# Kernel optimization log

Measured on AMD Instinct MI355X. Metric: run time of the kernel, lower is better.

Reference implementation:

```python
import jax, jax.numpy as jnp
import numpy as np

N = 20000
E = 320000
IN = 256
H = 4
C = 64
NEG_SLOPE = 0.2


def setup_inputs() -> dict:
    key = jax.random.key(0)
    ks = jax.random.split(key, 12)
    HC = H * C

    def w(k, shape, fan_in):
        return jax.random.normal(k, shape, dtype=jnp.float32) / np.sqrt(fan_in)

    x = jax.random.normal(ks[0], (N, IN), dtype=jnp.float32)
    edge_index = jax.random.randint(ks[1], (2, E), 0, N, dtype=jnp.int64)
    return {
        "x": x,
        "edge_index": edge_index,
        "Wl1": w(ks[2], (IN, HC), IN),
        "Wr1": w(ks[3], (IN, HC), IN),
        "att1": w(ks[4], (H, C), C),
        "b1": jnp.zeros((HC,), dtype=jnp.float32),
        "Wl2": w(ks[5], (HC, HC), HC),
        "Wr2": w(ks[6], (HC, HC), HC),
        "att2": w(ks[7], (H, C), C),
        "b2": jnp.zeros((HC,), dtype=jnp.float32),
        "Wfc": w(ks[8], (HC, 2), HC),
        "bfc": jnp.zeros((2,), dtype=jnp.float32),
    }


def _gatv2(x, src, dst, Wl, Wr, att, b):
    """GATv2Conv (concat=True, share_weights=False), inference (no dropout)."""
    n = x.shape[0]
    xl = (x @ Wl).reshape(n, H, C)  # source-side projection
    xr = (x @ Wr).reshape(n, H, C)  # target-side projection
    # per-edge GATv2 score: a^T LeakyReLU(xl_j + xr_i)
    e = jax.nn.leaky_relu(xl[src] + xr[dst], NEG_SLOPE)      # [E, H, C]
    score = jnp.einsum("ehc,hc->eh", e, att)                 # [E, H]
    # segment softmax over incoming edges of each target node
    smax = jax.ops.segment_max(score, dst, num_segments=n)   # [N, H]
    ex = jnp.exp(score - smax[dst])
    denom = jax.ops.segment_sum(ex, dst, num_segments=n)     # [N, H]
    alpha = ex / denom[dst]                                  # [E, H]
    # scatter-aggregate messages (source projections weighted by alpha)
    out = jax.ops.segment_sum(alpha[:, :, None] * xl[src], dst, num_segments=n)
    return out.reshape(n, H * C) + b


def reference(x, edge_index, Wl1, Wr1, att1, b1, Wl2, Wr2, att2, b2, Wfc, bfc):
    n = x.shape[0]
    # add_self_loops=True (PyG default)
    loop = jnp.arange(n, dtype=edge_index.dtype)
    src = jnp.concatenate([edge_index[0], loop])
    dst = jnp.concatenate([edge_index[1], loop])

    h = _gatv2(x, src, dst, Wl1, Wr1, att1, b1)
    h = jax.nn.relu(h)
    h = _gatv2(h, src, dst, Wl2, Wr2, att2, b2)
    h = jax.nn.relu(h)
    g = jnp.mean(h, axis=0, keepdims=True)  # [1, H*C]
    return g @ Wfc + bfc                    # [1, 2]
```

## Files before the change

kernel.cpp:

```cpp
#include <hip/hip_runtime.h>
#include <hip/hip_bf16.h>
#include <math.h>

#define Nn 20000
#define Ee 320000
#define INF_ 256
#define Hh 4
#define Cc 64
#define HC 256
#define NEG_SLOPE 0.2f

using frag16 = __attribute__((ext_vector_type(8))) short;
using f32x4  = __attribute__((ext_vector_type(4))) float;

__device__ __forceinline__ void async16(const void* g, void* l) {
    __builtin_amdgcn_global_load_lds(
        (const __attribute__((address_space(1))) unsigned int*)g,
        (__attribute__((address_space(3))) unsigned int*)l,
        16, 0, 0);
}


__global__ void init_deg(int* deg, int n) {
    int i = blockIdx.x * blockDim.x + threadIdx.x;
    if (i < n) deg[i] = 1;
}

__global__ void hist_kernel(const int* __restrict__ dst, int ne, int* deg) {
    int e = blockIdx.x * blockDim.x + threadIdx.x;
    if (e < ne) atomicAdd(&deg[dst[e]], 1);
}

__global__ __launch_bounds__(256) void scan1(const int* __restrict__ deg,
                                             int* __restrict__ excl,
                                             int* __restrict__ bsum, int n) {
    int tid = threadIdx.x;
    int gid = blockIdx.x * 256 + tid;
    int lane = tid & 63;
    int v = (gid < n) ? deg[gid] : 0;
    int x = v;
    #pragma unroll
    for (int off = 1; off < 64; off <<= 1) {
        int y = __shfl_up(x, off, 64);
        if (lane >= off) x += y;
    }
    __shared__ int wsum[4];
    if (lane == 63) wsum[tid >> 6] = x;
    __syncthreads();
    int wadd = 0;
    for (int w = 0; w < (tid >> 6); ++w) wadd += wsum[w];
    int incl = x + wadd;
    if (gid < n) excl[gid] = incl - v;
    if (tid == 255) bsum[blockIdx.x] = incl;
}

__global__ void scan2(const int* __restrict__ bsum, int* __restrict__ boff, int nb) {
    int lane = threadIdx.x;
    int carry = 0;
    for (int base = 0; base < nb; base += 64) {
        int i = base + lane;
        int v = (i < nb) ? bsum[i] : 0;
        int x = v;
        #pragma unroll
        for (int off = 1; off < 64; off <<= 1) {
            int y = __shfl_up(x, off, 64);
            if (lane >= off) x += y;
        }
        if (i < nb) boff[i] = carry + x - v;
        carry += __shfl(x, 63, 64);
    }
    if (lane == 0) boff[nb] = carry;
}

__global__ void scan_add(int* __restrict__ row_start, int* __restrict__ cursor,
                         const int* __restrict__ boff, int n, int nb) {
    int gid = blockIdx.x * blockDim.x + threadIdx.x;
    if (gid < n) {
        int v = row_start[gid] + boff[gid >> 8];
        row_start[gid] = v;
        cursor[gid] = v;
    }
    if (gid == n) row_start[n] = boff[nb];
}

__global__ void scatter_kernel(const int* __restrict__ src, const int* __restrict__ dst,
                               int ne, int n, int* cursor, int* colx) {
    int e = blockIdx.x * blockDim.x + threadIdx.x;
    if (e < ne) {
        int d = dst[e];
        int pos = atomicAdd(&cursor[d], 1);
        colx[pos] = src[e];
    } else if (e < ne + n) {
        int node = e - ne;
        int pos = atomicAdd(&cursor[node], 1);
        colx[pos] = node;
    }
}


__device__ inline unsigned short bf16rn(float f) {
    unsigned u = __float_as_uint(f);
    unsigned r = (u + 0x7FFFu + ((u >> 16) & 1u)) >> 16;
    return (unsigned short)r;
}

__device__ inline void split1(float v, short& h, short& l) {
    unsigned short hh = bf16rn(v);
    float back = __uint_as_float(((unsigned)hh) << 16);
    unsigned short ll = bf16rn(v - back);
    h = (short)hh; l = (short)ll;
}

__device__ __forceinline__ float4 bf4_to_f4(ushort4 u) {
    return make_float4(__uint_as_float((unsigned)u.x << 16),
                       __uint_as_float((unsigned)u.y << 16),
                       __uint_as_float((unsigned)u.z << 16),
                       __uint_as_float((unsigned)u.w << 16));
}

__global__ __launch_bounds__(256) void split_kernel(const float* __restrict__ in,
                                                    short* __restrict__ hi,
                                                    short* __restrict__ lo, int n4) {
    int i = blockIdx.x * blockDim.x + threadIdx.x;
    if (i >= n4) return;
    float4 v = ((const float4*)in)[i];
    short4 h, l;
    split1(v.x, h.x, l.x);
    split1(v.y, h.y, l.y);
    split1(v.z, h.z, l.z);
    split1(v.w, h.w, l.w);
    ((short4*)hi)[i] = h;
    ((short4*)lo)[i] = l;
}

__global__ __launch_bounds__(256) void wsplit_all(const float* __restrict__ Wl1,
                                                  const float* __restrict__ Wr1,
                                                  const float* __restrict__ Wl2,
                                                  const float* __restrict__ Wr2,
                                                  short* __restrict__ WhT1,
                                                  short* __restrict__ WlT1,
                                                  short* __restrict__ WhT2,
                                                  short* __restrict__ WlT2) {
    int b = blockIdx.x;
    int n = b & 255;
    int k = threadIdx.x;
    const float* W = (b < 256) ? Wl1 : (b < 512) ? Wr1 : (b < 768) ? Wl2 : Wr2;
    short* Wh = (b < 512) ? WhT1 : WhT2;
    short* Wl = (b < 512) ? WlT1 : WlT2;
    int col = b & 511;
    float v = W[k * 256 + n];
    short h, l;
    split1(v, h, l);
    Wh[col * 256 + k] = h;
    Wl[col * 256 + k] = l;
}


__global__ __launch_bounds__(256, 4) void mfma_gemm(const short* __restrict__ Ah,
                                                    const short* __restrict__ Al,
                                                    const short* __restrict__ WhT,
                                                    const short* __restrict__ WlT,
                                                    unsigned short* __restrict__ XLh,
                                                    float* __restrict__ XR) {
    __shared__ short BsH[64 * 256];
    __shared__ short BsL[64 * 256];

    int tid = threadIdx.x;
    int wave = tid >> 6, lane = tid & 63;
    int quad = lane >> 4, lc = lane & 15;

    int v = blockIdx.x;
    int p = (v & 7) * 157 + (v >> 3);
    int rowt = p >> 3;
    int colg = p & 7;
    int bm = rowt * 128;
    int cbase = (colg * 64) & 255;

    {
        int cl0 = wave * 2 + (lane >> 5);
        int kcs = (lane & 31) ^ (cl0 & 7);
        const short* srcH = WhT + (size_t)(colg * 64 + cl0) * HC + kcs * 8;
        const short* srcL = WlT + (size_t)(colg * 64 + cl0) * HC + kcs * 8;
        short* dstH = &BsH[wave * 512];
        short* dstL = &BsL[wave * 512];
        #pragma unroll
        for (int r = 0; r < 8; ++r) {
            async16(srcH + (size_t)r * 8 * HC, dstH + r * 2048);
            async16(srcL + (size_t)r * 8 * HC, dstL + r * 2048);
        }
    }

    int row0 = bm + wave * 32 + lc;
    int row1 = row0 + 16;
    int ca0 = (row0 < Nn) ? row0 : (Nn - 1);
    int ca1 = (row1 < Nn) ? row1 : (Nn - 1);
    const short* pa0h = Ah + (size_t)ca0 * HC + quad * 8;
    const short* pa1h = Ah + (size_t)ca1 * HC + quad * 8;
    const short* pa0l = Al + (size_t)ca0 * HC + quad * 8;
    const short* pa1l = Al + (size_t)ca1 * HC + quad * 8;

    __syncthreads();

    f32x4 acc[2][4] = {};
    #pragma unroll
    for (int c = 0; c < 8; ++c) {
        int k0 = c * 32;
        frag16 a0h = *(const frag16*)(pa0h + k0);
        frag16 a1h = *(const frag16*)(pa1h + k0);
        frag16 a0l = *(const frag16*)(pa0l + k0);
        frag16 a1l = *(const frag16*)(pa1l + k0);
        int sw = ((c * 4 + quad) ^ (lc & 7)) * 8;
        frag16 bh0 = *(const frag16*)&BsH[(0 * 16 + lc) * HC + sw];
        frag16 bh1 = *(const frag16*)&BsH[(1 * 16 + lc) * HC + sw];
        frag16 bh2 = *(const frag16*)&BsH[(2 * 16 + lc) * HC + sw];
        frag16 bh3 = *(const frag16*)&BsH[(3 * 16 + lc) * HC + sw];
        frag16 bl0 = *(const frag16*)&BsL[(0 * 16 + lc) * HC + sw];
        frag16 bl1 = *(const frag16*)&BsL[(1 * 16 + lc) * HC + sw];
        frag16 bl2 = *(const frag16*)&BsL[(2 * 16 + lc) * HC + sw];
        frag16 bl3 = *(const frag16*)&BsL[(3 * 16 + lc) * HC + sw];
        acc[0][0] = __builtin_amdgcn_mfma_f32_16x16x32_bf16(bh0, a0h, acc[0][0], 0, 0, 0);
        acc[1][0] = __builtin_amdgcn_mfma_f32_16x16x32_bf16(bh0, a1h, acc[1][0], 0, 0, 0);
        acc[0][1] = __builtin_amdgcn_mfma_f32_16x16x32_bf16(bh1, a0h, acc[0][1], 0, 0, 0);
        acc[1][1] = __builtin_amdgcn_mfma_f32_16x16x32_bf16(bh1, a1h, acc[1][1], 0, 0, 0);
        acc[0][2] = __builtin_amdgcn_mfma_f32_16x16x32_bf16(bh2, a0h, acc[0][2], 0, 0, 0);
        acc[1][2] = __builtin_amdgcn_mfma_f32_16x16x32_bf16(bh2, a1h, acc[1][2], 0, 0, 0);
        acc[0][3] = __builtin_amdgcn_mfma_f32_16x16x32_bf16(bh3, a0h, acc[0][3], 0, 0, 0);
        acc[1][3] = __builtin_amdgcn_mfma_f32_16x16x32_bf16(bh3, a1h, acc[1][3], 0, 0, 0);
        acc[0][0] = __builtin_amdgcn_mfma_f32_16x16x32_bf16(bh0, a0l, acc[0][0], 0, 0, 0);
        acc[1][0] = __builtin_amdgcn_mfma_f32_16x16x32_bf16(bh0, a1l, acc[1][0], 0, 0, 0);
        acc[0][1] = __builtin_amdgcn_mfma_f32_16x16x32_bf16(bh1, a0l, acc[0][1], 0, 0, 0);
        acc[1][1] = __builtin_amdgcn_mfma_f32_16x16x32_bf16(bh1, a1l, acc[1][1], 0, 0, 0);
        acc[0][2] = __builtin_amdgcn_mfma_f32_16x16x32_bf16(bh2, a0l, acc[0][2], 0, 0, 0);
        acc[1][2] = __builtin_amdgcn_mfma_f32_16x16x32_bf16(bh2, a1l, acc[1][2], 0, 0, 0);
        acc[0][3] = __builtin_amdgcn_mfma_f32_16x16x32_bf16(bh3, a0l, acc[0][3], 0, 0, 0);
        acc[1][3] = __builtin_amdgcn_mfma_f32_16x16x32_bf16(bh3, a1l, acc[1][3], 0, 0, 0);
        acc[0][0] = __builtin_amdgcn_mfma_f32_16x16x32_bf16(bl0, a0h, acc[0][0], 0, 0, 0);
        acc[1][0] = __builtin_amdgcn_mfma_f32_16x16x32_bf16(bl0, a1h, acc[1][0], 0, 0, 0);
        acc[0][1] = __builtin_amdgcn_mfma_f32_16x16x32_bf16(bl1, a0h, acc[0][1], 0, 0, 0);
        acc[1][1] = __builtin_amdgcn_mfma_f32_16x16x32_bf16(bl1, a1h, acc[1][1], 0, 0, 0);
        acc[0][2] = __builtin_amdgcn_mfma_f32_16x16x32_bf16(bl2, a0h, acc[0][2], 0, 0, 0);
        acc[1][2] = __builtin_amdgcn_mfma_f32_16x16x32_bf16(bl2, a1h, acc[1][2], 0, 0, 0);
        acc[0][3] = __builtin_amdgcn_mfma_f32_16x16x32_bf16(bl3, a0h, acc[0][3], 0, 0, 0);
        acc[1][3] = __builtin_amdgcn_mfma_f32_16x16x32_bf16(bl3, a1h, acc[1][3], 0, 0, 0);
    }

    #pragma unroll
    for (int mt = 0; mt < 2; ++mt) {
        int rw = bm + wave * 32 + mt * 16 + lc;
        if (rw >= Nn) continue;
        #pragma unroll
        for (int t = 0; t < 4; ++t) {
            int col0 = cbase + t * 16 + quad * 4;
            if (colg < 4) {
                ushort4 o;
                o.x = bf16rn(acc[mt][t][0]);
                o.y = bf16rn(acc[mt][t][1]);
                o.z = bf16rn(acc[mt][t][2]);
                o.w = bf16rn(acc[mt][t][3]);
                *(ushort4*)&XLh[(size_t)rw * HC + col0] = o;
            } else {
                *(f32x4*)&XR[(size_t)rw * HC + col0] = acc[mt][t];
            }
        }
    }
}


__device__ __forceinline__ float edge_score(const float4 v, const float4 xr,
                                            const float4 a06, const float4 a04) {
    float tx = v.x + xr.x, ty = v.y + xr.y, tz = v.z + xr.z, tw = v.w + xr.w;
    float p = a06.x * tx + a04.x * fabsf(tx);
    p += a06.y * ty + a04.y * fabsf(ty);
    p += a06.z * tz + a04.z * fabsf(tz);
    p += a06.w * tw + a04.w * fabsf(tw);
    p += __shfl_xor(p, 1, 64);
    p += __shfl_xor(p, 2, 64);
    p += __shfl_xor(p, 4, 64);
    p += __shfl_xor(p, 8, 64);
    return p;
}

__global__ __launch_bounds__(256) void gat_kernel(const ushort4* __restrict__ XL4,
                                                  const float4* __restrict__ XR4,
                                                  const int* __restrict__ row_start,
                                                  const int* __restrict__ colx,
                                                  const float4* __restrict__ att4,
                                                  const float4* __restrict__ bias4,
                                                  float4* __restrict__ Hout,
                                                  short4* __restrict__ Ahi,
                                                  short4* __restrict__ Alo,
                                                  int mode) {
    int wave = threadIdx.x >> 6, lane = threadIdx.x & 63;
    int node = blockIdx.x * 4 + wave;
    float4 xr = XR4[(size_t)node * 64 + lane];
    float4 a  = att4[lane];
    float4 a06 = make_float4(a.x * 0.6f, a.y * 0.6f, a.z * 0.6f, a.w * 0.6f);
    float4 a04 = make_float4(a.x * 0.4f, a.y * 0.4f, a.z * 0.4f, a.w * 0.4f);
    int e0 = __builtin_amdgcn_readfirstlane(row_start[node]);
    int e1 = __builtin_amdgcn_readfirstlane(row_start[node + 1]);
    float l0 = 0.f, l1 = 0.f;
    float4 acc0 = make_float4(0.f, 0.f, 0.f, 0.f);
    float4 acc1 = make_float4(0.f, 0.f, 0.f, 0.f);
    int npairs = (e1 - e0) >> 1;
    int e = e0;
    int s0 = 0, s1 = 0;
    if (npairs > 0) { s0 = colx[e]; s1 = colx[e + 1]; }
    for (int pp = 0; pp < npairs; ++pp) {
        int en = e + 2;
        int i0 = (en     < e1) ? en     : (e1 - 1);
        int i1 = (en + 1 < e1) ? en + 1 : (e1 - 1);
        int ns0 = colx[i0];
        int ns1 = colx[i1];
        ushort4 u0 = XL4[(size_t)s0 * 64 + lane];
        ushort4 u1 = XL4[(size_t)s1 * 64 + lane];
        float4 v0 = bf4_to_f4(u0);
        float4 v1 = bf4_to_f4(u1);
        float pe0 = __expf(edge_score(v0, xr, a06, a04));
        float pe1 = __expf(edge_score(v1, xr, a06, a04));
        l0 += pe0; l1 += pe1;
        acc0.x += pe0 * v0.x; acc0.y += pe0 * v0.y;
        acc0.z += pe0 * v0.z; acc0.w += pe0 * v0.w;
        acc1.x += pe1 * v1.x; acc1.y += pe1 * v1.y;
        acc1.z += pe1 * v1.z; acc1.w += pe1 * v1.w;
        s0 = ns0; s1 = ns1; e = en;
    }
    if (e < e1) {
        int st = colx[e];
        float4 v0 = bf4_to_f4(XL4[(size_t)st * 64 + lane]);
        float pe0 = __expf(edge_score(v0, xr, a06, a04));
        l0 += pe0;
        acc0.x += pe0 * v0.x; acc0.y += pe0 * v0.y;
        acc0.z += pe0 * v0.z; acc0.w += pe0 * v0.w;
    }
    float rl = 1.f / (l0 + l1);
    float4 b = bias4[lane];
    float4 o = make_float4(fmaxf((acc0.x + acc1.x) * rl + b.x, 0.f),
                           fmaxf((acc0.y + acc1.y) * rl + b.y, 0.f),
                           fmaxf((acc0.z + acc1.z) * rl + b.z, 0.f),
                           fmaxf((acc0.w + acc1.w) * rl + b.w, 0.f));
    size_t oidx = (size_t)node * 64 + lane;
    if (mode) {
        short4 h4, l4;
        split1(o.x, h4.x, l4.x);
        split1(o.y, h4.y, l4.y);
        split1(o.z, h4.z, l4.z);
        split1(o.w, h4.w, l4.w);
        Ahi[oidx] = h4;
        Alo[oidx] = l4;
    } else {
        Hout[oidx] = o;
    }
}


__global__ void zero_f(float* p, int n) {
    int i = blockIdx.x * blockDim.x + threadIdx.x;
    if (i < n) p[i] = 0.f;
}

__global__ __launch_bounds__(256) void colsum_kernel(const float* __restrict__ Hmat,
                                                     float* __restrict__ g, int n) {
    int ch = threadIdx.x;
    float s = 0.f;
    for (int r = blockIdx.x; r < n; r += gridDim.x)
        s += Hmat[(size_t)r * HC + ch];
    atomicAdd(&g[ch], s);
}

__global__ __launch_bounds__(256) void fc_kernel(const float* __restrict__ g,
                                                 const float* __restrict__ Wfc,
                                                 const float* __restrict__ bfc,
                                                 float* __restrict__ out, float invN) {
    int t = threadIdx.x;
    float gv = g[t] * invN;
    float p0 = gv * Wfc[2 * t];
    float p1 = gv * Wfc[2 * t + 1];
    #pragma unroll
    for (int off = 32; off > 0; off >>= 1) {
        p0 += __shfl_xor(p0, off, 64);
        p1 += __shfl_xor(p1, off, 64);
    }
    __shared__ float s0[4], s1[4];
    if ((t & 63) == 0) { s0[t >> 6] = p0; s1[t >> 6] = p1; }
    __syncthreads();
    if (t == 0) {
        out[0] = s0[0] + s0[1] + s0[2] + s0[3] + bfc[0];
        out[1] = s1[0] + s1[1] + s1[2] + s1[3] + bfc[1];
    }
}


extern "C" void kernel_launch(void* const* d_in, const int* in_sizes, int n_in,
                              void* d_out, int out_size, void* d_ws, size_t ws_size,
                              hipStream_t stream) {
    const float* x    = (const float*)d_in[0];
    const int*   eidx = (const int*)d_in[1];
    const float* Wl1  = (const float*)d_in[2];
    const float* Wr1  = (const float*)d_in[3];
    const float* att1 = (const float*)d_in[4];
    const float* b1   = (const float*)d_in[5];
    const float* Wl2  = (const float*)d_in[6];
    const float* Wr2  = (const float*)d_in[7];
    const float* att2 = (const float*)d_in[8];
    const float* b2   = (const float*)d_in[9];
    const float* Wfc  = (const float*)d_in[10];
    const float* bfc  = (const float*)d_in[11];
    float* out = (float*)d_out;

    const int* srcv = eidx;
    const int* dstv = eidx + Ee;

    size_t NHC = (size_t)Nn * HC;
    float* XR = (float*)d_ws;
    float* Hb = XR + NHC;
    float* g  = Hb + NHC;
    unsigned short* XLh = (unsigned short*)(g + HC);
    short* Ah   = (short*)(XLh + NHC);
    short* Al   = Ah + NHC;
    short* WhT1 = Al + NHC;
    short* WlT1 = WhT1 + 512 * 256;
    short* WhT2 = WlT1 + 512 * 256;
    short* WlT2 = WhT2 + 512 * 256;
    int* deg       = (int*)(WlT2 + 512 * 256);
    int* row_start = deg + Nn;
    int* cursor    = row_start + (Nn + 1);
    int* colx      = cursor + Nn;
    int* bsum      = colx + (Ee + Nn);
    int* boff      = bsum + 128;

    const int NB = (Nn + 255) / 256;
    const int N4 = (int)(NHC / 4);

    init_deg<<<(Nn + 255) / 256, 256, 0, stream>>>(deg, Nn);
    hist_kernel<<<(Ee + 255) / 256, 256, 0, stream>>>(dstv, Ee, deg);
    scan1<<<NB, 256, 0, stream>>>(deg, row_start, bsum, Nn);
    scan2<<<1, 64, 0, stream>>>(bsum, boff, NB);
    scan_add<<<(Nn + 256) / 256, 256, 0, stream>>>(row_start, cursor, boff, Nn, NB);
    scatter_kernel<<<(Ee + Nn + 255) / 256, 256, 0, stream>>>(srcv, dstv, Ee, Nn, cursor, colx);

    const int GB = 157 * 8;

    wsplit_all<<<1024, 256, 0, stream>>>(Wl1, Wr1, Wl2, Wr2, WhT1, WlT1, WhT2, WlT2);
    split_kernel<<<(N4 + 255) / 256, 256, 0, stream>>>(x, Ah, Al, N4);

    mfma_gemm<<<GB, 256, 0, stream>>>(Ah, Al, WhT1, WlT1, XLh, XR);
    gat_kernel<<<Nn / 4, 256, 0, stream>>>((const ushort4*)XLh, (const float4*)XR,
                                           row_start, colx, (const float4*)att1,
                                           (const float4*)b1, (float4*)Hb,
                                           (short4*)Ah, (short4*)Al, 1);

    mfma_gemm<<<GB, 256, 0, stream>>>(Ah, Al, WhT2, WlT2, XLh, XR);
    gat_kernel<<<Nn / 4, 256, 0, stream>>>((const ushort4*)XLh, (const float4*)XR,
                                           row_start, colx, (const float4*)att2,
                                           (const float4*)b2, (float4*)Hb,
                                           (short4*)Ah, (short4*)Al, 0);

    zero_f<<<1, 256, 0, stream>>>(g, HC);
    colsum_kernel<<<256, 256, 0, stream>>>(Hb, g, Nn);
    fc_kernel<<<1, 256, 0, stream>>>(g, Wfc, bfc, out, 1.0f / Nn);
}
```

Before: 283.4 us.

## Fuse CSR build into cooperative kernel, merge prep splits, fuse column-sum into GAT

Replaces six CSR-construction launches with one cooperative kernel that uses grid syncs. Merges the weight and input bf16 splitting into a single prep kernel, with a shared-memory transpose for the weights. The GEMM now reuses its loaded B tile across two row tiles, halving the grid. The second GAT layer reduces its output into 32 partial column sums with atomics instead of writing the full hidden matrix and running a separate colsum. These cut launch overhead and a large output write, at the cost of grid-sync latency and atomic contention.

Measured after the change: 802.7 us. 2.83x slower.

```diff
diff --git a/kernel.cpp b/kernel.cpp
--- a/kernel.cpp
+++ b/kernel.cpp
@@ -1,6 +1,9 @@
 #include <hip/hip_runtime.h>
 #include <hip/hip_bf16.h>
+#include <hip/hip_cooperative_groups.h>
 #include <math.h>
+
+namespace cg = cooperative_groups;
 
 #define Nn 20000
 #define Ee 320000
@@ -8,6 +11,7 @@
 #define Hh 4
 #define Cc 64
 #define HC 256
+#define NB_ 79
 #define NEG_SLOPE 0.2f
 
 using frag16 = __attribute__((ext_vector_type(8))) short;
@@ -21,83 +25,6 @@
 }
 
 
-__global__ void init_deg(int* deg, int n) {
-    int i = blockIdx.x * blockDim.x + threadIdx.x;
-    if (i < n) deg[i] = 1;
-}
-
-__global__ void hist_kernel(const int* __restrict__ dst, int ne, int* deg) {
-    int e = blockIdx.x * blockDim.x + threadIdx.x;
-    if (e < ne) atomicAdd(&deg[dst[e]], 1);
-}
-
-__global__ __launch_bounds__(256) void scan1(const int* __restrict__ deg,
-                                             int* __restrict__ excl,
-                                             int* __restrict__ bsum, int n) {
-    int tid = threadIdx.x;
-    int gid = blockIdx.x * 256 + tid;
-    int lane = tid & 63;
-    int v = (gid < n) ? deg[gid] : 0;
-    int x = v;
-    #pragma unroll
-    for (int off = 1; off < 64; off <<= 1) {
-        int y = __shfl_up(x, off, 64);
-        if (lane >= off) x += y;
-    }
-    __shared__ int wsum[4];
-    if (lane == 63) wsum[tid >> 6] = x;
-    __syncthreads();
-    int wadd = 0;
-    for (int w = 0; w < (tid >> 6); ++w) wadd += wsum[w];
-    int incl = x + wadd;
-    if (gid < n) excl[gid] = incl - v;
-    if (tid == 255) bsum[blockIdx.x] = incl;
-}
-
-__global__ void scan2(const int* __restrict__ bsum, int* __restrict__ boff, int nb) {
-    int lane = threadIdx.x;
-    int carry = 0;
-    for (int base = 0; base < nb; base += 64) {
-        int i = base + lane;
-        int v = (i < nb) ? bsum[i] : 0;
-        int x = v;
-        #pragma unroll
-        for (int off = 1; off < 64; off <<= 1) {
-            int y = __shfl_up(x, off, 64);
-            if (lane >= off) x += y;
-        }
-        if (i < nb) boff[i] = carry + x - v;
-        carry += __shfl(x, 63, 64);
-    }
-    if (lane == 0) boff[nb] = carry;
-}
-
-__global__ void scan_add(int* __restrict__ row_start, int* __restrict__ cursor,
-                         const int* __restrict__ boff, int n, int nb) {
-    int gid = blockIdx.x * blockDim.x + threadIdx.x;
-    if (gid < n) {
-        int v = row_start[gid] + boff[gid >> 8];
-        row_start[gid] = v;
-        cursor[gid] = v;
-    }
-    if (gid == n) row_start[n] = boff[nb];
-}
-
-__global__ void scatter_kernel(const int* __restrict__ src, const int* __restrict__ dst,
-                               int ne, int n, int* cursor, int* colx) {
-    int e = blockIdx.x * blockDim.x + threadIdx.x;
-    if (e < ne) {
-        int d = dst[e];
-        int pos = atomicAdd(&cursor[d], 1);
-        colx[pos] = src[e];
-    } else if (e < ne + n) {
-        int node = e - ne;
-        int pos = atomicAdd(&cursor[node], 1);
-        colx[pos] = node;
-    }
-}
-
-
 __device__ inline unsigned short bf16rn(float f) {
     unsigned u = __float_as_uint(f);
     unsigned r = (u + 0x7FFFu + ((u >> 16) & 1u)) >> 16;
@@ -118,41 +45,145 @@
                        __uint_as_float((unsigned)u.w << 16));
 }
 
-__global__ __launch_bounds__(256) void split_kernel(const float* __restrict__ in,
-                                                    short* __restrict__ hi,
-                                                    short* __restrict__ lo, int n4) {
-    int i = blockIdx.x * blockDim.x + threadIdx.x;
-    if (i >= n4) return;
-    float4 v = ((const float4*)in)[i];
-    short4 h, l;
-    split1(v.x, h.x, l.x);
-    split1(v.y, h.y, l.y);
-    split1(v.z, h.z, l.z);
-    split1(v.w, h.w, l.w);
-    ((short4*)hi)[i] = h;
-    ((short4*)lo)[i] = l;
-}
-
-__global__ __launch_bounds__(256) void wsplit_all(const float* __restrict__ Wl1,
-                                                  const float* __restrict__ Wr1,
-                                                  const float* __restrict__ Wl2,
-                                                  const float* __restrict__ Wr2,
-                                                  short* __restrict__ WhT1,
-                                                  short* __restrict__ WlT1,
-                                                  short* __restrict__ WhT2,
-                                                  short* __restrict__ WlT2) {
-    int b = blockIdx.x;
-    int n = b & 255;
-    int k = threadIdx.x;
-    const float* W = (b < 256) ? Wl1 : (b < 512) ? Wr1 : (b < 768) ? Wl2 : Wr2;
-    short* Wh = (b < 512) ? WhT1 : WhT2;
-    short* Wl = (b < 512) ? WlT1 : WlT2;
-    int col = b & 511;
-    float v = W[k * 256 + n];
-    short h, l;
-    split1(v, h, l);
-    Wh[col * 256 + k] = h;
-    Wl[col * 256 + k] = l;
+
+__global__ __launch_bounds__(256) void csr_coop(const int* __restrict__ dstv,
+                                                const int* __restrict__ srcv,
+                                                int* deg, int* row_start,
+                                                int* cursor, int* colx,
+                                                int* bsum, int* boff,
+                                                float* gpart) {
+    cg::grid_group grid = cg::this_grid();
+    int tid = threadIdx.x;
+    int gid0 = blockIdx.x * 256 + tid;
+    int stride = gridDim.x * 256;
+
+    for (int i = gid0; i < Nn; i += stride) deg[i] = 1;
+    for (int i = gid0; i < 32 * 256; i += stride) gpart[i] = 0.f;
+    grid.sync();
+
+    for (int e = gid0; e < Ee; e += stride) atomicAdd(&deg[dstv[e]], 1);
+    grid.sync();
+
+    if (blockIdx.x < NB_) {
+        int gid = blockIdx.x * 256 + tid;
+        int lane = tid & 63;
+        int v = (gid < Nn) ? deg[gid] : 0;
+        int x = v;
+        #pragma unroll
+        for (int off = 1; off < 64; off <<= 1) {
+            int y = __shfl_up(x, off, 64);
+            if (lane >= off) x += y;
+        }
+        __shared__ int wsum[4];
+        if (lane == 63) wsum[tid >> 6] = x;
+        __syncthreads();
+        int wadd = 0;
+        for (int w = 0; w < (tid >> 6); ++w) wadd += wsum[w];
+        int incl = x + wadd;
+        if (gid < Nn) row_start[gid] = incl - v;
+        if (tid == 255) bsum[blockIdx.x] = incl;
+    }
+    grid.sync();
+
+    if (blockIdx.x == 0 && tid < 64) {
+        int lane = tid;
+        int carry = 0;
+        for (int base = 0; base < NB_; base += 64) {
+            int i = base + lane;
+            int v = (i < NB_) ? bsum[i] : 0;
+            int x = v;
+            #pragma unroll
+            for (int off = 1; off < 64; off <<= 1) {
+                int y = __shfl_up(x, off, 64);
+                if (lane >= off) x += y;
+            }
+            if (i < NB_) boff[i] = carry + x - v;
+            carry += __shfl(x, 63, 64);
+        }
+        if (lane == 0) boff[NB_] = carry;
+    }
+    grid.sync();
+
+    for (int i = gid0; i < Nn; i += stride) {
+        int v = row_start[i] + boff[i >> 8];
+        row_start[i] = v;
+        cursor[i] = v;
+    }
+    if (gid0 == 0) row_start[Nn] = boff[NB_];
+    grid.sync();
+
+    for (int e = gid0; e < Ee + Nn; e += stride) {
+        if (e < Ee) {
+            int d = dstv[e];
+            int pos = atomicAdd(&cursor[d], 1);
+            colx[pos] = srcv[e];
+        } else {
+            int node = e - Ee;
+            int pos = atomicAdd(&cursor[node], 1);
+            colx[pos] = node;
+        }
+    }
+}
+
+
+__global__ __launch_bounds__(256) void prep(const float* __restrict__ x,
+                                            const float* __restrict__ Wl1,
+                                            const float* __restrict__ Wr1,
+                                            const float* __restrict__ Wl2,
+                                            const float* __restrict__ Wr2,
+                                            short* __restrict__ Ah,
+                                            short* __restrict__ Al,
+                                            short* __restrict__ WhT1,
+                                            short* __restrict__ WlT1,
+                                            short* __restrict__ WhT2,
+                                            short* __restrict__ WlT2,
+                                            int n4) {
+    __shared__ float T[64][65];
+    int b = blockIdx.x, tid = threadIdx.x;
+    if (b < 64) {
+        int m  = b >> 4;
+        int tr = (b >> 2) & 3;
+        int tc = b & 3;
+        const float* W = (m == 0) ? Wl1 : (m == 1) ? Wr1 : (m == 2) ? Wl2 : Wr2;
+        short* Wh = (m < 2) ? WhT1 : WhT2;
+        short* Wl = (m < 2) ? WlT1 : WlT2;
+        int colofs = (m & 1) * 256;
+        int lr = tid >> 4;
+        int lq = (tid & 15) * 4;
+        #pragma unroll
+        for (int it = 0; it < 4; ++it) {
+            int r = it * 16 + lr;
+            float4 v = *(const float4*)&W[(size_t)(tr * 64 + r) * 256 + tc * 64 + lq];
+            T[r][lq + 0] = v.x; T[r][lq + 1] = v.y;
+            T[r][lq + 2] = v.z; T[r][lq + 3] = v.w;
+        }
+        __syncthreads();
+        #pragma unroll
+        for (int it = 0; it < 4; ++it) {
+            int cl = it * 16 + lr;
+            int kl = (tid & 15) * 4;
+            short4 h, l;
+            split1(T[kl + 0][cl], h.x, l.x);
+            split1(T[kl + 1][cl], h.y, l.y);
+            split1(T[kl + 2][cl], h.z, l.z);
+            split1(T[kl + 3][cl], h.w, l.w);
+            size_t o = (size_t)(colofs + tc * 64 + cl) * 256 + tr * 64 + kl;
+            *(short4*)&Wh[o] = h;
+            *(short4*)&Wl[o] = l;
+        }
+    } else {
+        int i = (b - 64) * 256 + tid;
+        if (i < n4) {
+            float4 v = ((const float4*)x)[i];
+            short4 h, l;
+            split1(v.x, h.x, l.x);
+            split1(v.y, h.y, l.y);
+            split1(v.z, h.z, l.z);
+            split1(v.w, h.w, l.w);
+            ((short4*)Ah)[i] = h;
+            ((short4*)Al)[i] = l;
+        }
+    }
 }
 
 
@@ -170,10 +201,9 @@
     int quad = lane >> 4, lc = lane & 15;
 
     int v = blockIdx.x;
-    int p = (v & 7) * 157 + (v >> 3);
-    int rowt = p >> 3;
+    int p = (v & 7) * 79 + (v >> 3);
+    int j = p >> 3;
     int colg = p & 7;
-    int bm = rowt * 128;
     int cbase = (colg * 64) & 255;
 
     {
@@ -189,77 +219,83 @@
             async16(srcL + (size_t)r * 8 * HC, dstL + r * 2048);
         }
     }
-
-    int row0 = bm + wave * 32 + lc;
-    int row1 = row0 + 16;
-    int ca0 = (row0 < Nn) ? row0 : (Nn - 1);
-    int ca1 = (row1 < Nn) ? row1 : (Nn - 1);
-    const short* pa0h = Ah + (size_t)ca0 * HC + quad * 8;
-    const short* pa1h = Ah + (size_t)ca1 * HC + quad * 8;
-    const short* pa0l = Al + (size_t)ca0 * HC + quad * 8;
-    const short* pa1l = Al + (size_t)ca1 * HC + quad * 8;
-
     __syncthreads();
 
-    f32x4 acc[2][4] = {};
     #pragma unroll
-    for (int c = 0; c < 8; ++c) {
-        int k0 = c * 32;
-        frag16 a0h = *(const frag16*)(pa0h + k0);
-        frag16 a1h = *(const frag16*)(pa1h + k0);
-        frag16 a0l = *(const frag16*)(pa0l + k0);
-        frag16 a1l = *(const frag16*)(pa1l + k0);
-        int sw = ((c * 4 + quad) ^ (lc & 7)) * 8;
-        frag16 bh0 = *(const frag16*)&BsH[(0 * 16 + lc) * HC + sw];
-        frag16 bh1 = *(const frag16*)&BsH[(1 * 16 + lc) * HC + sw];
-        frag16 bh2 = *(const frag16*)&BsH[(2 * 16 + lc) * HC + sw];
-        frag16 bh3 = *(const frag16*)&BsH[(3 * 16 + lc) * HC + sw];
-        frag16 bl0 = *(const frag16*)&BsL[(0 * 16 + lc) * HC + sw];
-        frag16 bl1 = *(const frag16*)&BsL[(1 * 16 + lc) * HC + sw];
-        frag16 bl2 = *(const frag16*)&BsL[(2 * 16 + lc) * HC + sw];
-        frag16 bl3 = *(const frag16*)&BsL[(3 * 16 + lc) * HC + sw];
-        acc[0][0] = __builtin_amdgcn_mfma_f32_16x16x32_bf16(bh0, a0h, acc[0][0], 0, 0, 0);
-        acc[1][0] = __builtin_amdgcn_mfma_f32_16x16x32_bf16(bh0, a1h, acc[1][0], 0, 0, 0);
-        acc[0][1] = __builtin_amdgcn_mfma_f32_16x16x32_bf16(bh1, a0h, acc[0][1], 0, 0, 0);
-        acc[1][1] = __builtin_amdgcn_mfma_f32_16x16x32_bf16(bh1, a1h, acc[1][1], 0, 0, 0);
-        acc[0][2] = __builtin_amdgcn_mfma_f32_16x16x32_bf16(bh2, a0h, acc[0][2], 0, 0, 0);
-        acc[1][2] = __builtin_amdgcn_mfma_f32_16x16x32_bf16(bh2, a1h, acc[1][2], 0, 0, 0);
-        acc[0][3] = __builtin_amdgcn_mfma_f32_16x16x32_bf16(bh3, a0h, acc[0][3], 0, 0, 0);
-        acc[1][3] = __builtin_amdgcn_mfma_f32_16x16x32_bf16(bh3, a1h, acc[1][3], 0, 0, 0);
-        acc[0][0] = __builtin_amdgcn_mfma_f32_16x16x32_bf16(bh0, a0l, acc[0][0], 0, 0, 0);
-        acc[1][0] = __builtin_amdgcn_mfma_f32_16x16x32_bf16(bh0, a1l, acc[1][0], 0, 0, 0);
-        acc[0][1] = __builtin_amdgcn_mfma_f32_16x16x32_bf16(bh1, a0l, acc[0][1], 0, 0, 0);
-        acc[1][1] = __builtin_amdgcn_mfma_f32_16x16x32_bf16(bh1, a1l, acc[1][1], 0, 0, 0);
-        acc[0][2] = __builtin_amdgcn_mfma_f32_16x16x32_bf16(bh2, a0l, acc[0][2], 0, 0, 0);
-        acc[1][2] = __builtin_amdgcn_mfma_f32_16x16x32_bf16(bh2, a1l, acc[1][2], 0, 0, 0);
-        acc[0][3] = __builtin_amdgcn_mfma_f32_16x16x32_bf16(bh3, a0l, acc[0][3], 0, 0, 0);
-        acc[1][3] = __builtin_amdgcn_mfma_f32_16x16x32_bf16(bh3, a1l, acc[1][3], 0, 0, 0);
-        acc[0][0] = __builtin_amdgcn_mfma_f32_16x16x32_bf16(bl0, a0h, acc[0][0], 0, 0, 0);
-        acc[1][0] = __builtin_amdgcn_mfma_f32_16x16x32_bf16(bl0, a1h, acc[1][0], 0, 0, 0);
-        acc[0][1] = __builtin_amdgcn_mfma_f32_16x16x32_bf16(bl1, a0h, acc[0][1], 0, 0, 0);
-        acc[1][1] = __builtin_amdgcn_mfma_f32_16x16x32_bf16(bl1, a1h, acc[1][1], 0, 0, 0);
-        acc[0][2] = __builtin_amdgcn_mfma_f32_16x16x32_bf16(bl2, a0h, acc[0][2], 0, 0, 0);
-        acc[1][2] = __builtin_amdgcn_mfma_f32_16x16x32_bf16(bl2, a1h, acc[1][2], 0, 0, 0);
-        acc[0][3] = __builtin_amdgcn_mfma_f32_16x16x32_bf16(bl3, a0h, acc[0][3], 0, 0, 0);
-        acc[1][3] = __builtin_amdgcn_mfma_f32_16x16x32_bf16(bl3, a1h, acc[1][3], 0, 0, 0);
-    }
-
-    #pragma unroll
-    for (int mt = 0; mt < 2; ++mt) {
-        int rw = bm + wave * 32 + mt * 16 + lc;
-        if (rw >= Nn) continue;
-        #pragma unroll
-        for (int t = 0; t < 4; ++t) {
-            int col0 = cbase + t * 16 + quad * 4;
-            if (colg < 4) {
-                ushort4 o;
-                o.x = bf16rn(acc[mt][t][0]);
-                o.y = bf16rn(acc[mt][t][1]);
-                o.z = bf16rn(acc[mt][t][2]);
-                o.w = bf16rn(acc[mt][t][3]);
-                *(ushort4*)&XLh[(size_t)rw * HC + col0] = o;
-            } else {
-                *(f32x4*)&XR[(size_t)rw * HC + col0] = acc[mt][t];
+    for (int tt = 0; tt < 2; ++tt) {
+        int rowt = j + tt * 79;
+        if (rowt > 156) break;
+        int bm = rowt * 128;
+
+        int row0 = bm + wave * 32 + lc;
+        int row1 = row0 + 16;
+        int ca0 = (row0 < Nn) ? row0 : (Nn - 1);
+        int ca1 = (row1 < Nn) ? row1 : (Nn - 1);
+        const short* pa0h = Ah + (size_t)ca0 * HC + quad * 8;
+        const short* pa1h = Ah + (size_t)ca1 * HC + quad * 8;
+        const short* pa0l = Al + (size_t)ca0 * HC + quad * 8;
+        const short* pa1l = Al + (size_t)ca1 * HC + quad * 8;
+
+        f32x4 acc[2][4] = {};
+        #pragma unroll
+        for (int c = 0; c < 8; ++c) {
+            int k0 = c * 32;
+            frag16 a0h = *(const frag16*)(pa0h + k0);
+            frag16 a1h = *(const frag16*)(pa1h + k0);
+            frag16 a0l = *(const frag16*)(pa0l + k0);
+            frag16 a1l = *(const frag16*)(pa1l + k0);
+            int sw = ((c * 4 + quad) ^ (lc & 7)) * 8;
+            frag16 bh0 = *(const frag16*)&BsH[(0 * 16 + lc) * HC + sw];
+            frag16 bh1 = *(const frag16*)&BsH[(1 * 16 + lc) * HC + sw];
+            frag16 bh2 = *(const frag16*)&BsH[(2 * 16 + lc) * HC + sw];
+            frag16 bh3 = *(const frag16*)&BsH[(3 * 16 + lc) * HC + sw];
+            frag16 bl0 = *(const frag16*)&BsL[(0 * 16 + lc) * HC + sw];
+            frag16 bl1 = *(const frag16*)&BsL[(1 * 16 + lc) * HC + sw];
+            frag16 bl2 = *(const frag16*)&BsL[(2 * 16 + lc) * HC + sw];
+            frag16 bl3 = *(const frag16*)&BsL[(3 * 16 + lc) * HC + sw];
+            acc[0][0] = __builtin_amdgcn_mfma_f32_16x16x32_bf16(bh0, a0h, acc[0][0], 0, 0, 0);
+            acc[1][0] = __builtin_amdgcn_mfma_f32_16x16x32_bf16(bh0, a1h, acc[1][0], 0, 0, 0);
+            acc[0][1] = __builtin_amdgcn_mfma_f32_16x16x32_bf16(bh1, a0h, acc[0][1], 0, 0, 0);
+            acc[1][1] = __builtin_amdgcn_mfma_f32_16x16x32_bf16(bh1, a1h, acc[1][1], 0, 0, 0);
+            acc[0][2] = __builtin_amdgcn_mfma_f32_16x16x32_bf16(bh2, a0h, acc[0][2], 0, 0, 0);
+            acc[1][2] = __builtin_amdgcn_mfma_f32_16x16x32_bf16(bh2, a1h, acc[1][2], 0, 0, 0);
+            acc[0][3] = __builtin_amdgcn_mfma_f32_16x16x32_bf16(bh3, a0h, acc[0][3], 0, 0, 0);
+            acc[1][3] = __builtin_amdgcn_mfma_f32_16x16x32_bf16(bh3, a1h, acc[1][3], 0, 0, 0);
+            acc[0][0] = __builtin_amdgcn_mfma_f32_16x16x32_bf16(bh0, a0l, acc[0][0], 0, 0, 0);
+            acc[1][0] = __builtin_amdgcn_mfma_f32_16x16x32_bf16(bh0, a1l, acc[1][0], 0, 0, 0);
+            acc[0][1] = __builtin_amdgcn_mfma_f32_16x16x32_bf16(bh1, a0l, acc[0][1], 0, 0, 0);
+            acc[1][1] = __builtin_amdgcn_mfma_f32_16x16x32_bf16(bh1, a1l, acc[1][1], 0, 0, 0);
+            acc[0][2] = __builtin_amdgcn_mfma_f32_16x16x32_bf16(bh2, a0l, acc[0][2], 0, 0, 0);
+            acc[1][2] = __builtin_amdgcn_mfma_f32_16x16x32_bf16(bh2, a1l, acc[1][2], 0, 0, 0);
+            acc[0][3] = __builtin_amdgcn_mfma_f32_16x16x32_bf16(bh3, a0l, acc[0][3], 0, 0, 0);
+            acc[1][3] = __builtin_amdgcn_mfma_f32_16x16x32_bf16(bh3, a1l, acc[1][3], 0, 0, 0);
+            acc[0][0] = __builtin_amdgcn_mfma_f32_16x16x32_bf16(bl0, a0h, acc[0][0], 0, 0, 0);
+            acc[1][0] = __builtin_amdgcn_mfma_f32_16x16x32_bf16(bl0, a1h, acc[1][0], 0, 0, 0);
+            acc[0][1] = __builtin_amdgcn_mfma_f32_16x16x32_bf16(bl1, a0h, acc[0][1], 0, 0, 0);
+            acc[1][1] = __builtin_amdgcn_mfma_f32_16x16x32_bf16(bl1, a1h, acc[1][1], 0, 0, 0);
+            acc[0][2] = __builtin_amdgcn_mfma_f32_16x16x32_bf16(bl2, a0h, acc[0][2], 0, 0, 0);
+            acc[1][2] = __builtin_amdgcn_mfma_f32_16x16x32_bf16(bl2, a1h, acc[1][2], 0, 0, 0);
+            acc[0][3] = __builtin_amdgcn_mfma_f32_16x16x32_bf16(bl3, a0h, acc[0][3], 0, 0, 0);
+            acc[1][3] = __builtin_amdgcn_mfma_f32_16x16x32_bf16(bl3, a1h, acc[1][3], 0, 0, 0);
+        }
+
+        #pragma unroll
+        for (int mt = 0; mt < 2; ++mt) {
+            int rw = bm + wave * 32 + mt * 16 + lc;
+            if (rw >= Nn) continue;
+            #pragma unroll
+            for (int t = 0; t < 4; ++t) {
+                int col0 = cbase + t * 16 + quad * 4;
+                if (colg < 4) {
+                    ushort4 o;
+                    o.x = bf16rn(acc[mt][t][0]);
+                    o.y = bf16rn(acc[mt][t][1]);
+                    o.z = bf16rn(acc[mt][t][2]);
+                    o.w = bf16rn(acc[mt][t][3]);
+                    *(ushort4*)&XLh[(size_t)rw * HC + col0] = o;
+                } else {
+                    *(f32x4*)&XR[(size_t)rw * HC + col0] = acc[mt][t];
+                }
             }
         }
     }
@@ -286,10 +322,11 @@
                                                   const int* __restrict__ colx,
                                                   const float4* __restrict__ att4,
                                                   const float4* __restrict__ bias4,
-                                                  float4* __restrict__ Hout,
+                                                  float* __restrict__ gpart,
                                                   short4* __restrict__ Ahi,
                                                   short4* __restrict__ Alo,
                                                   int mode) {
+    __shared__ float4 sred[4][64];
     int wave = threadIdx.x >> 6, lane = threadIdx.x & 63;
     int node = blockIdx.x * 4 + wave;
     float4 xr = XR4[(size_t)node * 64 + lane];
@@ -338,41 +375,45 @@
                            fmaxf((acc0.y + acc1.y) * rl + b.y, 0.f),
                            fmaxf((acc0.z + acc1.z) * rl + b.z, 0.f),
                            fmaxf((acc0.w + acc1.w) * rl + b.w, 0.f));
-    size_t oidx = (size_t)node * 64 + lane;
     if (mode) {
         short4 h4, l4;
         split1(o.x, h4.x, l4.x);
         split1(o.y, h4.y, l4.y);
         split1(o.z, h4.z, l4.z);
         split1(o.w, h4.w, l4.w);
+        size_t oidx = (size_t)node * 64 + lane;
         Ahi[oidx] = h4;
         Alo[oidx] = l4;
     } else {
-        Hout[oidx] = o;
-    }
-}
-
-
-__global__ void zero_f(float* p, int n) {
-    int i = blockIdx.x * blockDim.x + threadIdx.x;
-    if (i < n) p[i] = 0.f;
-}
-
-__global__ __launch_bounds__(256) void colsum_kernel(const float* __restrict__ Hmat,
-                                                     float* __restrict__ g, int n) {
-    int ch = threadIdx.x;
-    float s = 0.f;
-    for (int r = blockIdx.x; r < n; r += gridDim.x)
-        s += Hmat[(size_t)r * HC + ch];
-    atomicAdd(&g[ch], s);
-}
-
-__global__ __launch_bounds__(256) void fc_kernel(const float* __restrict__ g,
+        sred[wave][lane] = o;
+        __syncthreads();
+        if (threadIdx.x < 64) {
+            int l = threadIdx.x;
+            float4 s = sred[0][l];
+            float4 s1v = sred[1][l], s2v = sred[2][l], s3v = sred[3][l];
+            s.x += s1v.x + s2v.x + s3v.x;
+            s.y += s1v.y + s2v.y + s3v.y;
+            s.z += s1v.z + s2v.z + s3v.z;
+            s.w += s1v.w + s2v.w + s3v.w;
+            float* gp = gpart + (blockIdx.x & 31) * 256 + l * 4;
+            atomicAdd(gp + 0, s.x);
+            atomicAdd(gp + 1, s.y);
+            atomicAdd(gp + 2, s.z);
+            atomicAdd(gp + 3, s.w);
+        }
+    }
+}
+
+
+__global__ __launch_bounds__(256) void fc_kernel(const float* __restrict__ gpart,
                                                  const float* __restrict__ Wfc,
                                                  const float* __restrict__ bfc,
                                                  float* __restrict__ out, float invN) {
     int t = threadIdx.x;
-    float gv = g[t] * invN;
+    float s = 0.f;
+    #pragma unroll
+    for (int k = 0; k < 32; ++k) s += gpart[k * 256 + t];
+    float gv = s * invN;
     float p0 = gv * Wfc[2 * t];
     float p1 = gv * Wfc[2 * t + 1];
     #pragma unroll
@@ -412,9 +453,8 @@
 
     size_t NHC = (size_t)Nn * HC;
     float* XR = (float*)d_ws;
-    float* Hb = XR + NHC;
-    float* g  = Hb + NHC;
-    unsigned short* XLh = (unsigned short*)(g + HC);
+    float* gpart = XR + NHC;
+    unsigned short* XLh = (unsigned short*)(gpart + 32 * 256);
     short* Ah   = (short*)(XLh + NHC);
     short* Al   = Ah + NHC;
     short* WhT1 = Al + NHC;
@@ -428,34 +468,32 @@
     int* bsum      = colx + (Ee + Nn);
     int* boff      = bsum + 128;
 
-    const int NB = (Nn + 255) / 256;
     const int N4 = (int)(NHC / 4);
 
-    init_deg<<<(Nn + 255) / 256, 256, 0, stream>>>(deg, Nn);
-    hist_kernel<<<(Ee + 255) / 256, 256, 0, stream>>>(dstv, Ee, deg);
-    scan1<<<NB, 256, 0, stream>>>(deg, row_start, bsum, Nn);
-    scan2<<<1, 64, 0, stream>>>(bsum, boff, NB);
-    scan_add<<<(Nn + 256) / 256, 256, 0, stream>>>(row_start, cursor, boff, Nn, NB);
-    scatter_kernel<<<(Ee + Nn + 255) / 256, 256, 0, stream>>>(srcv, dstv, Ee, Nn, cursor, colx);
-
-    const int GB = 157 * 8;
-
-    wsplit_all<<<1024, 256, 0, stream>>>(Wl1, Wr1, Wl2, Wr2, WhT1, WlT1, WhT2, WlT2);
-    split_kernel<<<(N4 + 255) / 256, 256, 0, stream>>>(x, Ah, Al, N4);
+    prep<<<64 + (N4 + 255) / 256, 256, 0, stream>>>(x, Wl1, Wr1, Wl2, Wr2,
+                                                    Ah, Al, WhT1, WlT1, WhT2, WlT2, N4);
+
+    {
+        void* cargs[] = {(void*)&dstv, (void*)&srcv, (void*)&deg, (void*)&row_start,
+                         (void*)&cursor, (void*)&colx, (void*)&bsum, (void*)&boff,
+                         (void*)&gpart};
+        hipLaunchCooperativeKernel((const void*)csr_coop, dim3(1024), dim3(256),
+                                   cargs, 0, stream);
+    }
+
+    const int GB = 8 * 79;
 
     mfma_gemm<<<GB, 256, 0, stream>>>(Ah, Al, WhT1, WlT1, XLh, XR);
     gat_kernel<<<Nn / 4, 256, 0, stream>>>((const ushort4*)XLh, (const float4*)XR,
                                            row_start, colx, (const float4*)att1,
-                                           (const float4*)b1, (float4*)Hb,
+                                           (const float4*)b1, gpart,
                                            (short4*)Ah, (short4*)Al, 1);
 
     mfma_gemm<<<GB, 256, 0, stream>>>(Ah, Al, WhT2, WlT2, XLh, XR);
     gat_kernel<<<Nn / 4, 256, 0, stream>>>((const ushort4*)XLh, (const float4*)XR,
                                            row_start, colx, (const float4*)att2,
-                                           (const float4*)b2, (float4*)Hb,
+                                           (const float4*)b2, gpart,
                                            (short4*)Ah, (short4*)Al, 0);
 
-    zero_f<<<1, 256, 0, stream>>>(g, HC);
-    colsum_kernel<<<256, 256, 0, stream>>>(Hb, g, Nn);
-    fc_kernel<<<1, 256, 0, stream>>>(g, Wfc, bfc, out, 1.0f / Nn);
-}
+    fc_kernel<<<1, 256, 0, stream>>>(gpart, Wfc, bfc, out, 1.0f / Nn);
+}
```
